# Optimization experiments

Measured on AMD Instinct MI355X. Metric: run time of the kernel, lower is better.

## Reference

```python
import jax, jax.numpy as jnp
import numpy as np

NUM_HEADS = 4
LN_EPS = 1e-5
L2_EPS = 1e-12


def setup_inputs() -> dict:
    key = jax.random.key(0)
    ks = jax.random.split(key, 10)
    B, L, D, Hd = 256, 197, 768, 512
    dh = Hd // NUM_HEADS  # 128
    NC = 1000
    sc = lambda k, shape, s: jax.random.normal(k, shape, jnp.float32) * s
    return {
        "cls_token": jax.random.normal(ks[0], (B, D), jnp.float32),
        "x": jax.random.normal(ks[1], (B, L, D), jnp.float32),
        "proj_w": sc(ks[2], (D, Hd), 0.02),
        "proj_b": jnp.zeros((Hd,), jnp.float32),
        "ln_g": jnp.ones((dh,), jnp.float32),
        "ln_b": jnp.zeros((dh,), jnp.float32),
        "conv1_w": sc(ks[3], (3, 3, 3, 3), 0.2),
        "conv2_w": sc(ks[4], (3, 3, 3, 3), 0.2),
        "cls1_w": sc(ks[5], (D, NC), 0.02),
        "cls1_b": jnp.zeros((NC,), jnp.float32),
        "cls2_w": sc(ks[6], (2883, NC), 0.02),
        "cls2_b": jnp.zeros((NC,), jnp.float32),
    }


def reference(cls_token, x, proj_w, proj_b, ln_g, ln_b, conv1_w, conv2_w,
              cls1_w, cls1_b, cls2_w, cls2_b):
    B, L, D = x.shape
    dh = ln_g.shape[0]
    # proj on patch tokens (drop cls at position 0)
    xp = x[:, 1:, :] @ proj_w + proj_b            # (B, 196, 512)
    Lp = xp.shape[1]
    H = xp.shape[2] // dh
    heads = xp.reshape(B, Lp, H, dh).transpose(2, 0, 1, 3)  # (H, B, Lp, dh)
    # LayerNorm over last dim (eps=1e-5, biased var, affine)
    mu = heads.mean(-1, keepdims=True)
    var = heads.var(-1, keepdims=True)
    hn = (heads - mu) * jax.lax.rsqrt(var + LN_EPS) * ln_g + ln_b
    # Covariance._remove_mean: adaptive_avg_pool2d on (B, dh, Lp) -> mean over BOTH dh and Lp per sample
    hn = hn - hn.mean(axis=(2, 3), keepdims=True)
    # 'near' cross-covariances between adjacent heads, all pairs batched
    x1, x2 = hn[:-1], hn[1:]                      # (H-1, B, Lp, dh)
    cov = jnp.einsum('pbnd,pbne->pbde', x1, x2) / Lp  # (H-1, B, dh, dh)
    # L2 normalize over dim=2 (row axis of each dh x dh map), F.normalize eps
    nrm = jnp.sqrt(jnp.sum(cov * cov, axis=2, keepdims=True))
    cov = cov / jnp.maximum(nrm, L2_EPS)
    cov = cov.transpose(1, 0, 2, 3)               # (B, 3, 128, 128)
    conv = lambda z, w: jax.lax.conv_general_dilated(
        z, w, (2, 2), 'VALID', dimension_numbers=('NCHW', 'OIHW', 'NCHW'))
    z = conv(cov, conv1_w)                        # (B, 3, 63, 63)
    z = jax.nn.gelu(z, approximate=False)
    z = conv(z, conv2_w)                          # (B, 3, 31, 31)
    flat = z.reshape(B, -1)                       # (B, 2883)
    out = ((cls_token @ cls1_w + cls1_b) + (flat @ cls2_w + cls2_b)) / 2
    return out
```

## Files before the change

kernel.cpp:

```cpp
#include <hip/hip_runtime.h>
#include <hip/hip_bf16.h>
#include <cstdint>

typedef __bf16 bf16_t;
typedef __bf16 bf16x4 __attribute__((ext_vector_type(4)));
typedef __bf16 bf16x8 __attribute__((ext_vector_type(8)));
typedef float floatx4 __attribute__((ext_vector_type(4)));

#define LNEPS 1e-5f

__device__ inline void async_copy16(const bf16_t* g, bf16_t* l) {
    __builtin_amdgcn_global_load_lds((const __attribute__((address_space(1))) void*)g,
                                     (__attribute__((address_space(3))) void*)l,
                                     16, 0, 0);
}

__global__ __launch_bounds__(256)
void k_cvt_x(const float* __restrict__ x, bf16_t* __restrict__ xbf) {
    const int vid = blockIdx.x * 256 + threadIdx.x;
    const int row = vid / 96;
    const int kv  = vid - row * 96;
    const int b = row / 196, l = row - (row / 196) * 196;
    const float* src = x + ((b * 197 + l + 1) * 96 + kv) * 8;
    const floatx4 f0 = *(const floatx4*)src;
    const floatx4 f1 = *(const floatx4*)(src + 4);
    bf16x8 o;
#pragma unroll
    for (int e = 0; e < 4; e++) { o[e] = (bf16_t)f0[e]; o[e+4] = (bf16_t)f1[e]; }
    *(bf16x8*)(xbf + vid * 8) = o;
}

__global__ __launch_bounds__(256)
void k_transpose_w(const float* __restrict__ w, bf16_t* __restrict__ wt) {
    __shared__ bf16_t tile[32][33];
    const int bx = blockIdx.x;
    const int by = blockIdx.y;
    const int tx = threadIdx.x & 31, ty = threadIdx.x >> 5;
    for (int i = ty; i < 32; i += 8)
        tile[i][tx] = (bf16_t)w[(by*32 + i)*512 + bx*32 + tx];
    __syncthreads();
    for (int i = ty; i < 32; i += 8)
        wt[(bx*32 + i)*768 + by*32 + tx] = tile[tx][i];
}

__global__ __launch_bounds__(256, 4)
void k_proj_ln(const bf16_t* __restrict__ xbf, const bf16_t* __restrict__ wt,
               const float* __restrict__ pb, const float* __restrict__ lng,
               const float* __restrict__ lnb, bf16_t* __restrict__ hn)
{
    __shared__ bf16_t As[128*32];
    __shared__ bf16_t Bs[128*32];

    const int t = threadIdx.x;
    const int lane = t & 63;
    const int w = t >> 6;
    const int q = lane >> 4;
    const int c = lane & 15;
    const int h = blockIdx.y;
    const int m0 = blockIdx.x * 128;

    const int srow  = t >> 2;
    const int skoff = (t & 3) * 8;
    const bf16_t* ag0 = xbf + (m0 + srow) * 768 + skoff;
    const bf16_t* ag1 = ag0 + 64*768;
    const bf16_t* bg0 = wt + (h*128 + srow)*768 + skoff;
    const bf16_t* bg1 = bg0 + 64*768;

    floatx4 acc[2][8];
#pragma unroll
    for (int i = 0; i < 2; i++)
#pragma unroll
        for (int j = 0; j < 8; j++)
#pragma unroll
            for (int r = 0; r < 4; r++) acc[i][j][r] = 0.f;

    for (int k0 = 0; k0 < 768; k0 += 32) {
        __syncthreads();
        async_copy16(ag0 + k0, &As[t*8]);
        async_copy16(ag1 + k0, &As[2048 + t*8]);
        async_copy16(bg0 + k0, &Bs[t*8]);
        async_copy16(bg1 + k0, &Bs[2048 + t*8]);
        __syncthreads();
        bf16x8 af[2], bfr[8];
#pragma unroll
        for (int i = 0; i < 2; i++)
            af[i] = *(const bf16x8*)&As[(w*32 + i*16 + c)*32 + q*8];
#pragma unroll
        for (int j = 0; j < 8; j++)
            bfr[j] = *(const bf16x8*)&Bs[(j*16 + c)*32 + q*8];
#pragma unroll
        for (int i = 0; i < 2; i++)
#pragma unroll
            for (int j = 0; j < 8; j++)
                acc[i][j] = __builtin_amdgcn_mfma_f32_16x16x32_bf16(af[i], bfr[j], acc[i][j], 0, 0, 0);
    }

    float bias[8], gg[8], bb[8];
#pragma unroll
    for (int j = 0; j < 8; j++) {
        const int d = j*16 + c;
        bias[j] = pb[h*128 + d];
        gg[j]   = lng[d];
        bb[j]   = lnb[d];
    }
#pragma unroll
    for (int i = 0; i < 2; i++) {
#pragma unroll
        for (int r = 0; r < 4; r++) {
            float s = 0.f, s2 = 0.f;
#pragma unroll
            for (int j = 0; j < 8; j++) {
                const float v = acc[i][j][r] + bias[j];
                acc[i][j][r] = v;
                s += v; s2 += v*v;
            }
#pragma unroll
            for (int o = 1; o < 16; o <<= 1) { s += __shfl_xor(s, o); s2 += __shfl_xor(s2, o); }
            const float mu = s * (1.f/128.f);
            const float ms = s2 * (1.f/128.f);
            const float rstd = rsqrtf(ms - mu*mu + LNEPS);
            const int gm = m0 + w*32 + i*16 + q*4 + r;
            const int bI = gm / 196, l = gm - bI*196;
            bf16_t* dst = hn + (((h*256 + bI)*196 + l) << 7);
#pragma unroll
            for (int j = 0; j < 8; j++) {
                const float v = (acc[i][j][r] - mu)*rstd*gg[j] + bb[j];
                dst[j*16 + c] = (bf16_t)v;
            }
        }
    }
}

__global__ __launch_bounds__(256)
void k_colsum(const bf16_t* __restrict__ hn, float* __restrict__ colsum)
{
    __shared__ float tmp[2][128];
    const int t = threadIdx.x;
    const int d = t & 127, half = t >> 7;
    const bf16_t* S = hn + ((long)blockIdx.x * 196 << 7);
    float s = 0.f;
    const int n0 = half * 98;
    for (int n = 0; n < 98; n++) s += (float)S[((n0 + n) << 7) + d];
    tmp[half][d] = s;
    __syncthreads();
    if (t < 128) colsum[(blockIdx.x << 7) + t] = tmp[0][t] + tmp[1][t];
}

__global__ __launch_bounds__(256, 2)
void k_cov(const bf16_t* __restrict__ hn, const float* __restrict__ colsum,
           float* __restrict__ cov)
{
    __shared__ bf16_t x1s[128*40];
    __shared__ bf16_t x2s[128*40];
    __shared__ float rs1[128], rs2[128];
    __shared__ float colsq[2][128];
    __shared__ float nrm_inv[128];
    __shared__ float mu_s[2];

    const int t = threadIdx.x;
    const int lane = t & 63;
    const int wv = t >> 6;
    const int wr = wv >> 1, wc = wv & 1;
    const int q = lane >> 4;
    const int c = lane & 15;
    const int b = blockIdx.x;
    const int p = blockIdx.y;

    const bf16_t* X1 = hn + (((p*256 + b)*196) << 7);
    const bf16_t* X2 = hn + ((((p+1)*256 + b)*196) << 7);

    if (t < 128) rs1[t] = colsum[((p*256 + b) << 7) + t];
    else         rs2[t & 127] = colsum[(((p+1)*256 + b) << 7) + (t & 127)];
    __syncthreads();
    if (wv == 0) {
        float s = rs1[lane] + rs1[lane + 64];
#pragma unroll
        for (int o = 1; o < 64; o <<= 1) s += __shfl_xor(s, o);
        if (lane == 0) mu_s[0] = s * (1.f/(196.f*128.f));
    } else if (wv == 1) {
        float s = rs2[lane] + rs2[lane + 64];
#pragma unroll
        for (int o = 1; o < 64; o <<= 1) s += __shfl_xor(s, o);
        if (lane == 0) mu_s[1] = s * (1.f/(196.f*128.f));
    }

    floatx4 acc[4][4];
#pragma unroll
    for (int i = 0; i < 4; i++)
#pragma unroll
        for (int j = 0; j < 4; j++)
#pragma unroll
            for (int r = 0; r < 4; r++) acc[i][j][r] = 0.f;

    const int nl = t >> 3;
    const int d0 = (t & 7) * 16;

    for (int n0 = 0; n0 < 224; n0 += 32) {
        __syncthreads();
        const int n = n0 + nl;
        bf16x8 va, vb, wa, wb;
        if (n < 196) {
            const bf16_t* s1 = X1 + (n << 7) + d0;
            const bf16_t* s2 = X2 + (n << 7) + d0;
            va = *(const bf16x8*)s1;
            vb = *(const bf16x8*)(s1 + 8);
            wa = *(const bf16x8*)s2;
            wb = *(const bf16x8*)(s2 + 8);
        } else {
#pragma unroll
            for (int e = 0; e < 8; e++) {
                va[e] = (bf16_t)0.f; vb[e] = (bf16_t)0.f;
                wa[e] = (bf16_t)0.f; wb[e] = (bf16_t)0.f;
            }
        }
#pragma unroll
        for (int e = 0; e < 8; e++) {
            x1s[(d0 + e)*40 + nl]     = va[e];
            x1s[(d0 + 8 + e)*40 + nl] = vb[e];
            x2s[(d0 + e)*40 + nl]     = wa[e];
            x2s[(d0 + 8 + e)*40 + nl] = wb[e];
        }
        __syncthreads();
        bf16x8 af[4], bfr[4];
#pragma unroll
        for (int i = 0; i < 4; i++)
            af[i] = *(const bf16x8*)&x1s[(wr*64 + i*16 + c)*40 + q*8];
#pragma unroll
        for (int j = 0; j < 4; j++)
            bfr[j] = *(const bf16x8*)&x2s[(wc*64 + j*16 + c)*40 + q*8];
#pragma unroll
        for (int i = 0; i < 4; i++)
#pragma unroll
            for (int j = 0; j < 4; j++)
                acc[i][j] = __builtin_amdgcn_mfma_f32_16x16x32_bf16(af[i], bfr[j], acc[i][j], 0, 0, 0);
    }

    const float mu1 = mu_s[0], mu2 = mu_s[1];
    const float invL = 1.f/196.f;
    float csq[4] = {0.f, 0.f, 0.f, 0.f};
#pragma unroll
    for (int i = 0; i < 4; i++)
#pragma unroll
        for (int j = 0; j < 4; j++)
#pragma unroll
            for (int r = 0; r < 4; r++) {
                const int d = wr*64 + i*16 + q*4 + r;
                const int e = wc*64 + j*16 + c;
                const float v = acc[i][j][r]*invL - mu2*rs1[d]*invL - mu1*rs2[e]*invL + mu1*mu2;
                acc[i][j][r] = v;
                csq[j] += v*v;
            }
#pragma unroll
    for (int j = 0; j < 4; j++) {
        float s = csq[j];
        s += __shfl_xor(s, 16);
        s += __shfl_xor(s, 32);
        csq[j] = s;
    }
    if (q == 0) {
#pragma unroll
        for (int j = 0; j < 4; j++) colsq[wr][wc*64 + j*16 + c] = csq[j];
    }
    __syncthreads();
    if (t < 128) {
        const float nr = sqrtf(colsq[0][t] + colsq[1][t]);
        nrm_inv[t] = 1.f / fmaxf(nr, 1e-12f);
    }
    __syncthreads();
    float* dst = cov + ((long)b*3 + p)*16384;
#pragma unroll
    for (int i = 0; i < 4; i++)
#pragma unroll
        for (int j = 0; j < 4; j++) {
            const int e = wc*64 + j*16 + c;
            const float ni = nrm_inv[e];
#pragma unroll
            for (int r = 0; r < 4; r++) {
                const int d = wr*64 + i*16 + q*4 + r;
                dst[(d << 7) + e] = acc[i][j][r] * ni;
            }
        }
}

__global__ __launch_bounds__(256)
void k_convs(const float* __restrict__ cov, const float* __restrict__ w1,
             const float* __restrict__ w2, bf16_t* __restrict__ Xb)
{
    __shared__ float Z[3*3969];
    __shared__ float W1s[81];
    __shared__ float W2s[81];
    const int t = threadIdx.x, b = blockIdx.x;
    if (t < 81) { W1s[t] = w1[t]; W2s[t] = w2[t]; }
    __syncthreads();
    const float* C = cov + (long)b*3*16384;
    for (int idx = t; idx < 3*3969; idx += 256) {
        const int o = idx / 3969, rem = idx - o*3969;
        const int y = rem / 63, xx = rem - y*63;
        float a = 0.f;
#pragma unroll
        for (int i = 0; i < 3; i++) {
            const float* Ci = C + i*16384 + (2*y)*128 + 2*xx;
            const float* Wi = &W1s[o*27 + i*9];
            a += Ci[0]*Wi[0]   + Ci[1]*Wi[1]   + Ci[2]*Wi[2]
               + Ci[128]*Wi[3] + Ci[129]*Wi[4] + Ci[130]*Wi[5]
               + Ci[256]*Wi[6] + Ci[257]*Wi[7] + Ci[258]*Wi[8];
        }
        Z[idx] = 0.5f*a*(1.0f + erff(a*0.70710678118654752f));
    }
    __syncthreads();
    for (int idx = t; idx < 2883; idx += 256) {
        const int o = idx / 961, rem = idx - o*961;
        const int y = rem / 31, xx = rem - y*31;
        float a = 0.f;
#pragma unroll
        for (int i = 0; i < 3; i++) {
            const float* Zi = Z + i*3969 + (2*y)*63 + 2*xx;
            const float* Wi = &W2s[(o*3+i)*9];
            a += Zi[0]*Wi[0]   + Zi[1]*Wi[1]   + Zi[2]*Wi[2]
               + Zi[63]*Wi[3]  + Zi[64]*Wi[4]  + Zi[65]*Wi[5]
               + Zi[126]*Wi[6] + Zi[127]*Wi[7] + Zi[128]*Wi[8];
        }
        Xb[(long)b*3712 + 768 + idx] = (bf16_t)a;
    }
}

__global__ __launch_bounds__(256)
void k_cvt_cls(const float* __restrict__ cls, bf16_t* __restrict__ Xb)
{
    const int t = threadIdx.x, b = blockIdx.x;
    for (int k = t; k < 768; k += 256)
        Xb[b*3712 + k] = (bf16_t)cls[b*768 + k];
    if (t < 61) Xb[b*3712 + 3651 + t] = (bf16_t)0.f;
}

__global__ __launch_bounds__(256)
void k_cvt_w(const float* __restrict__ W1, const float* __restrict__ W2,
             bf16_t* __restrict__ Wb)
{
    __shared__ bf16_t tile[32][33];
    const int k0 = blockIdx.x * 32;
    const int n0 = blockIdx.y * 32;
    const int tx = threadIdx.x & 31, ty = threadIdx.x >> 5;
    for (int i = ty; i < 32; i += 8) {
        const int k = k0 + i, n = n0 + tx;
        float v = 0.f;
        if (n < 1000 && k < 3651)
            v = (k < 768) ? W1[k*1000 + n] : W2[(k-768)*1000 + n];
        tile[i][tx] = (bf16_t)v;
    }
    __syncthreads();
    for (int i = ty; i < 32; i += 8)
        Wb[(n0 + i)*3712 + k0 + tx] = tile[tx][i];
}

__global__ __launch_bounds__(256, 2)
void k_gemm_cls(const bf16_t* __restrict__ Xb, const bf16_t* __restrict__ Wb,
                float* __restrict__ partial)
{
    __shared__ bf16_t As[128*32];
    __shared__ bf16_t Bs[128*32];

    const int t = threadIdx.x;
    const int lane = t & 63;
    const int wv = t >> 6;
    const int wr = wv >> 1, wc = wv & 1;
    const int q = lane >> 4;
    const int c = lane & 15;
    const int nt = blockIdx.x;
    const int mt = blockIdx.y;
    const int sp = blockIdx.z;

    const int srow  = t >> 2;
    const int skoff = (t & 3) * 8;
    const int m0 = mt * 128, n0 = nt * 128;
    const int kbase = sp * 928;
    const bf16_t* ag0 = Xb + (m0 + srow) * 3712 + kbase + skoff;
    const bf16_t* ag1 = Xb + (m0 + srow + 64) * 3712 + kbase + skoff;
    const bf16_t* bg0 = Wb + (n0 + srow) * 3712 + kbase + skoff;
    const bf16_t* bg1 = Wb + (n0 + srow + 64) * 3712 + kbase + skoff;

    floatx4 acc[4][4];
#pragma unroll
    for (int i = 0; i < 4; i++)
#pragma unroll
        for (int j = 0; j < 4; j++)
#pragma unroll
            for (int r = 0; r < 4; r++) acc[i][j][r] = 0.f;

    for (int k0 = 0; k0 < 928; k0 += 32) {
        __syncthreads();
        async_copy16(ag0 + k0, &As[t*8]);
        async_copy16(ag1 + k0, &As[2048 + t*8]);
        async_copy16(bg0 + k0, &Bs[t*8]);
        async_copy16(bg1 + k0, &Bs[2048 + t*8]);
        __syncthreads();
        bf16x8 af[4], bfr[4];
#pragma unroll
        for (int i = 0; i < 4; i++)
            af[i] = *(const bf16x8*)&As[(wr*64 + i*16 + c)*32 + q*8];
#pragma unroll
        for (int j = 0; j < 4; j++)
            bfr[j] = *(const bf16x8*)&Bs[(wc*64 + j*16 + c)*32 + q*8];
#pragma unroll
        for (int i = 0; i < 4; i++)
#pragma unroll
            for (int j = 0; j < 4; j++)
                acc[i][j] = __builtin_amdgcn_mfma_f32_16x16x32_bf16(af[i], bfr[j], acc[i][j], 0, 0, 0);
    }

    float* base = partial + ((long)sp*256 + m0)*1024 + n0;
#pragma unroll
    for (int i = 0; i < 4; i++)
#pragma unroll
        for (int r = 0; r < 4; r++) {
            const int row = wr*64 + i*16 + q*4 + r;
#pragma unroll
            for (int j = 0; j < 4; j++)
                base[row*1024 + wc*64 + j*16 + c] = acc[i][j][r];
        }
}

__global__ __launch_bounds__(256)
void k_cls_fin(const float* __restrict__ partial, const float* __restrict__ b1,
               const float* __restrict__ b2, float* __restrict__ out)
{
    const int idx = blockIdx.x * 256 + threadIdx.x;
    const int m = idx / 1000, n = idx - m*1000;
    float s = partial[(m)*1024 + n] + partial[(256 + m)*1024 + n]
            + partial[(512 + m)*1024 + n] + partial[(768 + m)*1024 + n];
    out[idx] = 0.5f*(s + b1[n] + b2[n]);
}

extern "C" void kernel_launch(void* const* d_in, const int* in_sizes, int n_in,
                              void* d_out, int out_size, void* d_ws, size_t ws_size,
                              hipStream_t stream) {
    const float* cls = (const float*)d_in[0];
    const float* x   = (const float*)d_in[1];
    const float* pw  = (const float*)d_in[2];
    const float* pb  = (const float*)d_in[3];
    const float* lng = (const float*)d_in[4];
    const float* lnb = (const float*)d_in[5];
    const float* c1w = (const float*)d_in[6];
    const float* c2w = (const float*)d_in[7];
    const float* w1  = (const float*)d_in[8];
    const float* b1  = (const float*)d_in[9];
    const float* w2  = (const float*)d_in[10];
    const float* b2  = (const float*)d_in[11];

    char* ws = (char*)d_ws;
    bf16_t* hn    = (bf16_t*)(ws);
    bf16_t* xbf   = (bf16_t*)(ws + 51380224ull);
    bf16_t* wt    = (bf16_t*)(ws + 128450560ull);
    float*  covb  = (float*) (ws + 51380224ull);
    float*  csum  = (float*) (ws + 129236992ull);
    bf16_t* Xb    = (bf16_t*)(ws + 129761280ull);
    bf16_t* Wb    = (bf16_t*)(ws + 131661824ull);
    float*  part  = (float*) (ws + 139264000ull);
    float*  out   = (float*)d_out;

    k_transpose_w<<<dim3(16, 24), 256, 0, stream>>>(pw, wt);
    k_cvt_x<<<18816, 256, 0, stream>>>(x, xbf);
    k_cvt_cls<<<256, 256, 0, stream>>>(cls, Xb);
    k_cvt_w<<<dim3(116, 32), 256, 0, stream>>>(w1, w2, Wb);
    k_proj_ln<<<dim3(392, 4), 256, 0, stream>>>(xbf, wt, pb, lng, lnb, hn);
    k_colsum<<<1024, 256, 0, stream>>>(hn, csum);
    k_cov<<<dim3(256, 3), 256, 0, stream>>>(hn, csum, covb);
    k_convs<<<256, 256, 0, stream>>>(covb, c1w, c2w, Xb);
    k_gemm_cls<<<dim3(8, 2, 4), 256, 0, stream>>>(Xb, Wb, part);
    k_cls_fin<<<1000, 256, 0, stream>>>(part, b1, b2, out);
}
```

Baseline: 445.3 us.

## Fuse fp32-to-bf16 conversion of x into projection GEMM with register-prefetched double buffer

After: 519.4 us. 16.6% more time.

```diff
diff --git a/kernel.cpp b/kernel.cpp
--- a/kernel.cpp
+++ b/kernel.cpp
@@ -13,21 +13,6 @@
     __builtin_amdgcn_global_load_lds((const __attribute__((address_space(1))) void*)g,
                                      (__attribute__((address_space(3))) void*)l,
                                      16, 0, 0);
-}
-
-__global__ __launch_bounds__(256)
-void k_cvt_x(const float* __restrict__ x, bf16_t* __restrict__ xbf) {
-    const int vid = blockIdx.x * 256 + threadIdx.x;
-    const int row = vid / 96;
-    const int kv  = vid - row * 96;
-    const int b = row / 196, l = row - (row / 196) * 196;
-    const float* src = x + ((b * 197 + l + 1) * 96 + kv) * 8;
-    const floatx4 f0 = *(const floatx4*)src;
-    const floatx4 f1 = *(const floatx4*)(src + 4);
-    bf16x8 o;
-#pragma unroll
-    for (int e = 0; e < 4; e++) { o[e] = (bf16_t)f0[e]; o[e+4] = (bf16_t)f1[e]; }
-    *(bf16x8*)(xbf + vid * 8) = o;
 }
 
 __global__ __launch_bounds__(256)
@@ -43,28 +28,29 @@
         wt[(bx*32 + i)*768 + by*32 + tx] = tile[tx][i];
 }
 
-__global__ __launch_bounds__(256, 4)
-void k_proj_ln(const bf16_t* __restrict__ xbf, const bf16_t* __restrict__ wt,
+__global__ __launch_bounds__(256, 3)
+void k_proj_ln(const float* __restrict__ x, const bf16_t* __restrict__ wt,
                const float* __restrict__ pb, const float* __restrict__ lng,
                const float* __restrict__ lnb, bf16_t* __restrict__ hn)
 {
-    __shared__ bf16_t As[128*32];
-    __shared__ bf16_t Bs[128*32];
+    __shared__ bf16_t As[2][128*40];
 
     const int t = threadIdx.x;
     const int lane = t & 63;
     const int w = t >> 6;
     const int q = lane >> 4;
     const int c = lane & 15;
-    const int h = blockIdx.y;
-    const int m0 = blockIdx.x * 128;
-
-    const int srow  = t >> 2;
-    const int skoff = (t & 3) * 8;
-    const bf16_t* ag0 = xbf + (m0 + srow) * 768 + skoff;
-    const bf16_t* ag1 = ag0 + 64*768;
-    const bf16_t* bg0 = wt + (h*128 + srow)*768 + skoff;
-    const bf16_t* bg1 = bg0 + 64*768;
+    const int h = blockIdx.x;
+    const int m0 = blockIdx.y * 128;
+
+    const int arow = t >> 1;
+    const int ak   = (t & 1) * 16;
+    const int gr = m0 + arow;
+    const int bI0 = gr / 196, l0 = gr - bI0*196;
+    const float* ag = x + (size_t)(bI0*197 + l0 + 1)*768 + ak;
+    const int awoff = arow*40 + ak;
+
+    const bf16_t* bg = wt + (h*128 + c)*768 + q*8;
 
     floatx4 acc[2][8];
 #pragma unroll
@@ -74,25 +60,62 @@
 #pragma unroll
             for (int r = 0; r < 4; r++) acc[i][j][r] = 0.f;
 
-    for (int k0 = 0; k0 < 768; k0 += 32) {
-        __syncthreads();
-        async_copy16(ag0 + k0, &As[t*8]);
-        async_copy16(ag1 + k0, &As[2048 + t*8]);
-        async_copy16(bg0 + k0, &Bs[t*8]);
-        async_copy16(bg1 + k0, &Bs[2048 + t*8]);
-        __syncthreads();
-        bf16x8 af[2], bfr[8];
+    floatx4 pa0, pa1, pa2, pa3;
+    pa0 = *(const floatx4*)(ag + 0);
+    pa1 = *(const floatx4*)(ag + 4);
+    pa2 = *(const floatx4*)(ag + 8);
+    pa3 = *(const floatx4*)(ag + 12);
+    {
+        bf16x8 o0, o1;
+#pragma unroll
+        for (int e = 0; e < 4; e++) {
+            o0[e] = (bf16_t)pa0[e]; o0[e+4] = (bf16_t)pa1[e];
+            o1[e] = (bf16_t)pa2[e]; o1[e+4] = (bf16_t)pa3[e];
+        }
+        *(bf16x8*)&As[0][awoff]     = o0;
+        *(bf16x8*)&As[0][awoff + 8] = o1;
+    }
+    pa0 = *(const floatx4*)(ag + 32);
+    pa1 = *(const floatx4*)(ag + 36);
+    pa2 = *(const floatx4*)(ag + 40);
+    pa3 = *(const floatx4*)(ag + 44);
+    __syncthreads();
+
+    for (int it = 0; it < 24; ++it) {
+        const int k0 = it * 32;
+        const bf16_t* Acur = As[it & 1];
+        bf16x8 af[2];
 #pragma unroll
         for (int i = 0; i < 2; i++)
-            af[i] = *(const bf16x8*)&As[(w*32 + i*16 + c)*32 + q*8];
+            af[i] = *(const bf16x8*)&Acur[(w*32 + i*16 + c)*40 + q*8];
+        bf16x8 bfr[8];
 #pragma unroll
         for (int j = 0; j < 8; j++)
-            bfr[j] = *(const bf16x8*)&Bs[(j*16 + c)*32 + q*8];
+            bfr[j] = *(const bf16x8*)(bg + j*16*768 + k0);
+        if (it < 23) {
+            bf16x8 o0, o1;
+#pragma unroll
+            for (int e = 0; e < 4; e++) {
+                o0[e] = (bf16_t)pa0[e]; o0[e+4] = (bf16_t)pa1[e];
+                o1[e] = (bf16_t)pa2[e]; o1[e+4] = (bf16_t)pa3[e];
+            }
+            bf16_t* Anxt = As[(it + 1) & 1];
+            *(bf16x8*)&Anxt[awoff]     = o0;
+            *(bf16x8*)&Anxt[awoff + 8] = o1;
+            if (it < 22) {
+                const float* nxt = ag + k0 + 64;
+                pa0 = *(const floatx4*)(nxt + 0);
+                pa1 = *(const floatx4*)(nxt + 4);
+                pa2 = *(const floatx4*)(nxt + 8);
+                pa3 = *(const floatx4*)(nxt + 12);
+            }
+        }
 #pragma unroll
         for (int i = 0; i < 2; i++)
 #pragma unroll
             for (int j = 0; j < 8; j++)
                 acc[i][j] = __builtin_amdgcn_mfma_f32_16x16x32_bf16(af[i], bfr[j], acc[i][j], 0, 0, 0);
+        __syncthreads();
     }
 
     float bias[8], gg[8], bb[8];
@@ -449,7 +472,6 @@
 
     char* ws = (char*)d_ws;
     bf16_t* hn    = (bf16_t*)(ws);
-    bf16_t* xbf   = (bf16_t*)(ws + 51380224ull);
     bf16_t* wt    = (bf16_t*)(ws + 128450560ull);
     float*  covb  = (float*) (ws + 51380224ull);
     float*  csum  = (float*) (ws + 129236992ull);
@@ -459,10 +481,9 @@
     float*  out   = (float*)d_out;
 
     k_transpose_w<<<dim3(16, 24), 256, 0, stream>>>(pw, wt);
-    k_cvt_x<<<18816, 256, 0, stream>>>(x, xbf);
     k_cvt_cls<<<256, 256, 0, stream>>>(cls, Xb);
     k_cvt_w<<<dim3(116, 32), 256, 0, stream>>>(w1, w2, Wb);
-    k_proj_ln<<<dim3(392, 4), 256, 0, stream>>>(xbf, wt, pb, lng, lnb, hn);
+    k_proj_ln<<<dim3(4, 392), 256, 0, stream>>>(x, wt, pb, lng, lnb, hn);
     k_colsum<<<1024, 256, 0, stream>>>(hn, csum);
     k_cov<<<dim3(256, 3), 256, 0, stream>>>(hn, csum, covb);
     k_convs<<<256, 256, 0, stream>>>(covb, c1w, c2w, Xb);
```

## Fuse fp32-to-bf16 conversion of x into projection GEMM with register prefetch

Applied to the files above, without the earlier changes.

Measured after the change: 463.7 us. 4.1% more time.

```diff
diff --git a/kernel.cpp b/kernel.cpp
--- a/kernel.cpp
+++ b/kernel.cpp
@@ -13,21 +13,6 @@
     __builtin_amdgcn_global_load_lds((const __attribute__((address_space(1))) void*)g,
                                      (__attribute__((address_space(3))) void*)l,
                                      16, 0, 0);
-}
-
-__global__ __launch_bounds__(256)
-void k_cvt_x(const float* __restrict__ x, bf16_t* __restrict__ xbf) {
-    const int vid = blockIdx.x * 256 + threadIdx.x;
-    const int row = vid / 96;
-    const int kv  = vid - row * 96;
-    const int b = row / 196, l = row - (row / 196) * 196;
-    const float* src = x + ((b * 197 + l + 1) * 96 + kv) * 8;
-    const floatx4 f0 = *(const floatx4*)src;
-    const floatx4 f1 = *(const floatx4*)(src + 4);
-    bf16x8 o;
-#pragma unroll
-    for (int e = 0; e < 4; e++) { o[e] = (bf16_t)f0[e]; o[e+4] = (bf16_t)f1[e]; }
-    *(bf16x8*)(xbf + vid * 8) = o;
 }
 
 __global__ __launch_bounds__(256)
@@ -43,13 +28,13 @@
         wt[(bx*32 + i)*768 + by*32 + tx] = tile[tx][i];
 }
 
-__global__ __launch_bounds__(256, 4)
-void k_proj_ln(const bf16_t* __restrict__ xbf, const bf16_t* __restrict__ wt,
+__global__ __launch_bounds__(256, 3)
+void k_proj_ln(const float* __restrict__ x, const bf16_t* __restrict__ wt,
                const float* __restrict__ pb, const float* __restrict__ lng,
                const float* __restrict__ lnb, bf16_t* __restrict__ hn)
 {
-    __shared__ bf16_t As[128*32];
-    __shared__ bf16_t Bs[128*32];
+    __shared__ bf16_t As[128*72];
+    __shared__ bf16_t Bs[128*72];
 
     const int t = threadIdx.x;
     const int lane = t & 63;
@@ -59,12 +44,13 @@
     const int h = blockIdx.y;
     const int m0 = blockIdx.x * 128;
 
-    const int srow  = t >> 2;
-    const int skoff = (t & 3) * 8;
-    const bf16_t* ag0 = xbf + (m0 + srow) * 768 + skoff;
-    const bf16_t* ag1 = ag0 + 64*768;
-    const bf16_t* bg0 = wt + (h*128 + srow)*768 + skoff;
-    const bf16_t* bg1 = bg0 + 64*768;
+    const int srow  = t >> 1;
+    const int skoff = (t & 1) * 32;
+    const int gr = m0 + srow;
+    const int bI0 = gr / 196, l0 = gr - bI0*196;
+    const float*  agp = x  + (size_t)(bI0*197 + l0 + 1)*768 + skoff;
+    const bf16_t* bgp = wt + (size_t)(h*128 + srow)*768 + skoff;
+    const int woff = srow*72 + skoff;
 
     floatx4 acc[2][8];
 #pragma unroll
@@ -74,25 +60,54 @@
 #pragma unroll
             for (int r = 0; r < 4; r++) acc[i][j][r] = 0.f;
 
-    for (int k0 = 0; k0 < 768; k0 += 32) {
-        __syncthreads();
-        async_copy16(ag0 + k0, &As[t*8]);
-        async_copy16(ag1 + k0, &As[2048 + t*8]);
-        async_copy16(bg0 + k0, &Bs[t*8]);
-        async_copy16(bg1 + k0, &Bs[2048 + t*8]);
-        __syncthreads();
-        bf16x8 af[2], bfr[8];
-#pragma unroll
-        for (int i = 0; i < 2; i++)
-            af[i] = *(const bf16x8*)&As[(w*32 + i*16 + c)*32 + q*8];
-#pragma unroll
-        for (int j = 0; j < 8; j++)
-            bfr[j] = *(const bf16x8*)&Bs[(j*16 + c)*32 + q*8];
-#pragma unroll
-        for (int i = 0; i < 2; i++)
+    floatx4 pa[8];
+    bf16x8  pbv[4];
+#pragma unroll
+    for (int u = 0; u < 8; u++) pa[u] = *(const floatx4*)(agp + u*4);
+#pragma unroll
+    for (int u = 0; u < 4; u++) pbv[u] = *(const bf16x8*)(bgp + u*8);
+
+    for (int it = 0; it < 12; ++it) {
+        __syncthreads();
+        {
+            bf16x8 o[4];
+#pragma unroll
+            for (int u = 0; u < 4; u++)
+#pragma unroll
+                for (int e = 0; e < 4; e++) {
+                    o[u][e]   = (bf16_t)pa[2*u][e];
+                    o[u][e+4] = (bf16_t)pa[2*u+1][e];
+                }
+#pragma unroll
+            for (int u = 0; u < 4; u++) {
+                *(bf16x8*)&As[woff + u*8] = o[u];
+                *(bf16x8*)&Bs[woff + u*8] = pbv[u];
+            }
+        }
+        __syncthreads();
+        if (it < 11) {
+            const float*  an = agp + (it + 1)*64;
+            const bf16_t* bn = bgp + (it + 1)*64;
+#pragma unroll
+            for (int u = 0; u < 8; u++) pa[u] = *(const floatx4*)(an + u*4);
+#pragma unroll
+            for (int u = 0; u < 4; u++) pbv[u] = *(const bf16x8*)(bn + u*8);
+        }
+#pragma unroll
+        for (int kk = 0; kk < 2; ++kk) {
+            bf16x8 af[2], bfr[8];
+#pragma unroll
+            for (int i = 0; i < 2; i++)
+                af[i] = *(const bf16x8*)&As[(w*32 + i*16 + c)*72 + kk*32 + q*8];
 #pragma unroll
             for (int j = 0; j < 8; j++)
-                acc[i][j] = __builtin_amdgcn_mfma_f32_16x16x32_bf16(af[i], bfr[j], acc[i][j], 0, 0, 0);
+                bfr[j] = *(const bf16x8*)&Bs[(j*16 + c)*72 + kk*32 + q*8];
+#pragma unroll
+            for (int i = 0; i < 2; i++)
+#pragma unroll
+                for (int j = 0; j < 8; j++)
+                    acc[i][j] = __builtin_amdgcn_mfma_f32_16x16x32_bf16(af[i], bfr[j], acc[i][j], 0, 0, 0);
+        }
     }
 
     float bias[8], gg[8], bb[8];
@@ -449,7 +464,6 @@
 
     char* ws = (char*)d_ws;
     bf16_t* hn    = (bf16_t*)(ws);
-    bf16_t* xbf   = (bf16_t*)(ws + 51380224ull);
     bf16_t* wt    = (bf16_t*)(ws + 128450560ull);
     float*  covb  = (float*) (ws + 51380224ull);
     float*  csum  = (float*) (ws + 129236992ull);
@@ -459,10 +473,9 @@
     float*  out   = (float*)d_out;
 
     k_transpose_w<<<dim3(16, 24), 256, 0, stream>>>(pw, wt);
-    k_cvt_x<<<18816, 256, 0, stream>>>(x, xbf);
     k_cvt_cls<<<256, 256, 0, stream>>>(cls, Xb);
     k_cvt_w<<<dim3(116, 32), 256, 0, stream>>>(w1, w2, Wb);
-    k_proj_ln<<<dim3(392, 4), 256, 0, stream>>>(xbf, wt, pb, lng, lnb, hn);
+    k_proj_ln<<<dim3(392, 4), 256, 0, stream>>>(x, wt, pb, lng, lnb, hn);
     k_colsum<<<1024, 256, 0, stream>>>(hn, csum);
     k_cov<<<dim3(256, 3), 256, 0, stream>>>(hn, csum, covb);
     k_convs<<<256, 256, 0, stream>>>(covb, c1w, c2w, Xb);
```
